# Kernel tuning notes

Hardware: AMD Instinct MI355X
Metric: run time of the kernel (lower is better)

Reference implementation:

```python
import jax, jax.numpy as jnp
import numpy as np

S, V = 64, 32          # input scalar / vector multiplicities (64x0e + 32x1o)
MID_S, MID_V = 96, 96  # irreps_mid = 64x0e+32x0e + 64x1o+32x1o
NB = 10                # number_of_basis (radial edge scalars)
N_NODES, N_EDGES = 50000, 400000


def _fctp_attr(xs, xv, attr, Ws, Wv):
    # FullyConnectedTensorProduct(x, node_attr='1x0e'): per-irrep-block linear
    # mixing scaled by the scalar attr, path weight 1/sqrt(fan_in).
    os = (xs @ Ws) * attr * (1.0 / np.sqrt(xs.shape[1]))
    ov = jnp.einsum('nui,uk->nki', xv, Wv) * attr[..., None] * (1.0 / np.sqrt(xv.shape[1]))
    return os, ov


def _conv(ns, nv, attr, src, dst, sh, esc,
          Wsc_s, Wsc_v, Wl1_s, Wl1_v, Wfc1, Wfc2, Wl2_s, Wl2_v, Wa):
    # GraphConvolutionWithNodeAttrs: gather -> weighted e3nn TP -> scatter-mean
    N, E = ns.shape[0], src.shape[0]
    # radial MLP (e3nn FullyConnectedNet, silu) -> per-edge tp weights (192)
    h = jax.nn.silu(esc @ Wfc1 * (1.0 / np.sqrt(esc.shape[1])))
    w = h @ Wfc2 * (1.0 / np.sqrt(h.shape[1]))
    w1, w2, w3, w4 = w[:, :64], w[:, 64:128], w[:, 128:160], w[:, 160:192]
    sc_s, sc_v = _fctp_attr(ns, nv, attr, Wsc_s, Wsc_v)   # self connection
    hs, hv = _fctp_attr(ns, nv, attr, Wl1_s, Wl1_v)       # lin1
    gs, gv = hs[src], hv[src]                              # gather by edge_src
    sh0, shv = sh[:, 0:1], sh[:, 1:4]                      # 1x0e, 1x1o edge sh
    # 'uvu' instructions: (0e x 0e -> 0e), (1o x 1o -> 0e), (0e x 1o -> 1o), (1o x 0e -> 1o)
    m_s = jnp.concatenate([
        gs * sh0 * w1,                                                     # [E,64]
        jnp.einsum('evi,ei->ev', gv, shv) * (1.0 / np.sqrt(3.0)) * w4],   # [E,32]
        axis=1)                                                            # [E,96]
    m_v = jnp.concatenate([
        gs[:, :, None] * shv[:, None, :] * w2[:, :, None],  # [E,64,3]
        gv * sh0[:, :, None] * w3[:, :, None]],              # [E,32,3]
        axis=1)                                              # [E,96,3]
    # scatter with reduce='mean' onto destination nodes
    deg = jnp.maximum(jax.ops.segment_sum(jnp.ones((E,), ns.dtype), dst, num_segments=N), 1.0)
    Ms = jax.ops.segment_sum(m_s, dst, num_segments=N) / deg[:, None]
    Mv = jax.ops.segment_sum(m_v, dst, num_segments=N) / deg[:, None, None]
    alpha = (Ms @ Wa) * (1.0 / np.sqrt(MID_S)) * attr      # [N,1] (output_mask==1)
    os, ov = _fctp_attr(Ms, Mv, attr, Wl2_s, Wl2_v)        # lin2
    return sc_s + alpha * os, sc_v + alpha[..., None] * ov


def _forward(node_s, node_v, node_attr, edge_src, edge_dst, edge_sh, edge_scalars, p1, p2):
    s, v = _conv(node_s, node_v, node_attr, edge_src, edge_dst, edge_sh, edge_scalars, *p1)
    # Gate: 64 scalars (silu) | 32 gates (sigmoid) gating 32x1o vectors
    gs = jax.nn.silu(s[:, :64])
    v = v * jax.nn.sigmoid(s[:, 64:96])[:, :, None]
    s2, v2 = _conv(gs, v, node_attr, edge_src, edge_dst, edge_sh, edge_scalars, *p2)
    return jnp.concatenate([s2, v2.reshape(v2.shape[0], -1)], axis=1)  # [N,160]


def setup_inputs():
    ks = jax.random.split(jax.random.key(0), 32)
    N, E = N_NODES, N_EDGES
    g = lambda i, shape: jax.random.normal(ks[i], shape, jnp.float32)
    inp = {'node_s': g(0, (N, S)),
           'node_v': g(1, (N, V, 3)),
           'node_attr': jnp.ones((N, 1), jnp.float32),
           'edge_src': jax.random.randint(ks[2], (E,), 0, N),
           'edge_dst': jax.random.randint(ks[3], (E,), 0, N),
           'edge_sh': g(4, (E, 4)),
           'edge_scalars': jax.random.uniform(ks[5], (E, NB), jnp.float32)}
    dims = {1: (96, 32), 2: (64, 32)}  # layer1 conv out feeds gate; layer2 is final conv
    i = 6
    for L in (1, 2):
        o_s, o_v = dims[L]
        for name, shape in [('sc_s', (S, o_s)), ('sc_v', (V, o_v)), ('lin1_s', (S, S)),
                            ('lin1_v', (V, V)), ('fc1', (NB, 64)), ('fc2', (64, 192)),
                            ('lin2_s', (MID_S, o_s)), ('lin2_v', (MID_V, o_v)), ('alpha', (MID_S, 1))]:
            inp['l%d_%s' % (L, name)] = g(i, shape)
            i += 1
    return inp


def reference(node_s, node_v, node_attr, edge_src, edge_dst, edge_sh, edge_scalars,
              l1_sc_s, l1_sc_v, l1_lin1_s, l1_lin1_v, l1_fc1, l1_fc2, l1_lin2_s, l1_lin2_v, l1_alpha,
              l2_sc_s, l2_sc_v, l2_lin1_s, l2_lin1_v, l2_fc1, l2_fc2, l2_lin2_s, l2_lin2_v, l2_alpha):
    p1 = (l1_sc_s, l1_sc_v, l1_lin1_s, l1_lin1_v, l1_fc1, l1_fc2, l1_lin2_s, l1_lin2_v, l1_alpha)
    p2 = (l2_sc_s, l2_sc_v, l2_lin1_s, l2_lin1_v, l2_fc1, l2_fc2, l2_lin2_s, l2_lin2_v, l2_alpha)
    return _forward(node_s, node_v, node_attr, edge_src, edge_dst, edge_sh, edge_scalars, p1, p2)
```

## Files before the change

kernel.cpp:

```cpp
#include <hip/hip_runtime.h>
#include <hip/hip_bf16.h>

#define INV_SQRT10 0.31622776601683794f
#define INV_SQRT64 0.125f
#define INV_SQRT32 0.17677669529663687f
#define INV_SQRT96 0.10206207261596575f
#define INV_SQRT3  0.5773502691896258f

typedef __attribute__((ext_vector_type(4))) float f32x4;
typedef __attribute__((ext_vector_type(8))) short bf16x8;

__device__ __forceinline__ unsigned short f2bf(float x) {
    return __builtin_bit_cast(unsigned short, (__hip_bfloat16)x);
}
__device__ __forceinline__ float bf2f(unsigned short u) {
    union { unsigned u; float f; } v; v.u = ((unsigned)u) << 16;
    return v.f;
}

__global__ __launch_bounds__(256) void k_prep_nodes(
    const float* __restrict__ ns, const float* __restrict__ nv,
    const int* __restrict__ dst,
    unsigned short* __restrict__ xsb, unsigned short* __restrict__ xvpb,
    int* __restrict__ cnt, int N, int E)
{
    const int gid = blockIdx.x * 256 + threadIdx.x, gs = gridDim.x * 256;
    for (int i = gid; i < N * 64; i += gs) xsb[i] = f2bf(ns[i]);
    for (int i = gid; i < N * 96; i += gs) {
        const int n = i / 96, rem = i - n * 96;
        const int ic = rem >> 5, u = rem & 31;
        xvpb[i] = f2bf(nv[(size_t)n * 96 + u * 3 + ic]);
    }
    for (int i = gid; i < E; i += gs) atomicAdd(&cnt[dst[i]], 1);
}

template <int OS>
__global__ __launch_bounds__(256) void k_prep_w(
    const float* __restrict__ Wl1s, const float* __restrict__ Wscs,
    const float* __restrict__ Wl1v, const float* __restrict__ Wscv,
    const float* __restrict__ Wfc2,
    const float* __restrict__ W2s, const float* __restrict__ W2v,
    const float* __restrict__ Wa,
    unsigned short* __restrict__ wsb, unsigned short* __restrict__ wvb,
    unsigned short* __restrict__ wfb,
    unsigned short* __restrict__ wob, unsigned short* __restrict__ wv2b)
{
    constexpr int NC1 = 64 + OS;
    constexpr int PC1 = ((OS + 16 + 15) / 16) * 16;
    const int gid = blockIdx.x * 256 + threadIdx.x, gs = gridDim.x * 256;
    for (int i = gid; i < NC1 * 64; i += gs) {
        const int c = i >> 6, k = i & 63;
        const float v = (c < 64) ? Wl1s[k * 64 + c] : Wscs[k * OS + (c - 64)];
        wsb[i] = f2bf(v);
    }
    for (int i = gid; i < 64 * 32; i += gs) {
        const int c = i >> 5, u = i & 31;
        const float v = (c < 32) ? Wl1v[u * 32 + c] : Wscv[u * 32 + (c - 32)];
        wvb[i] = f2bf(v);
    }
    for (int i = gid; i < 192 * 64; i += gs) {
        const int c = i >> 6, k = i & 63;
        wfb[i] = f2bf(Wfc2[k * 192 + c]);
    }
    for (int i = gid; i < PC1 * 96; i += gs) {
        const int c = i / 96, u = i - c * 96;
        float v = 0.f;
        if (c < OS) v = W2s[u * OS + c];
        else if (c == OS) v = Wa[u];
        wob[i] = f2bf(v);
    }
    for (int i = gid; i < 32 * 96; i += gs) {
        const int c = i / 96, u = i - c * 96;
        wv2b[i] = f2bf(W2v[u * 32 + c]);
    }
}

__global__ __launch_bounds__(256) void k_scan1(const int* __restrict__ cnt,
                                               int* __restrict__ partial, int N)
{
    __shared__ int lds[256];
    const int t = threadIdx.x, i = blockIdx.x * 256 + t;
    int v = (i < N) ? cnt[i] : 0;
    lds[t] = v;
    __syncthreads();
    for (int off = 128; off > 0; off >>= 1) {
        if (t < off) lds[t] += lds[t + off];
        __syncthreads();
    }
    if (t == 0) partial[blockIdx.x] = lds[0];
}

__global__ __launch_bounds__(1024) void k_scan2(int* __restrict__ partial, int NB)
{
    __shared__ int lds[1024];
    const int t = threadIdx.x;
    int v = (t < NB) ? partial[t] : 0;
    lds[t] = v;
    __syncthreads();
    for (int off = 1; off < 1024; off <<= 1) {
        int w = (t >= off) ? lds[t - off] : 0;
        __syncthreads();
        lds[t] += w;
        __syncthreads();
    }
    if (t < NB) partial[t] = lds[t] - v;
}

__global__ __launch_bounds__(256) void k_scan3(const int* __restrict__ cnt,
                                               const int* __restrict__ partial,
                                               int* __restrict__ base, int N)
{
    __shared__ int lds[256];
    const int t = threadIdx.x, i = blockIdx.x * 256 + t;
    int v = (i < N) ? cnt[i] : 0;
    lds[t] = v;
    __syncthreads();
    for (int off = 1; off < 256; off <<= 1) {
        int w = (t >= off) ? lds[t - off] : 0;
        __syncthreads();
        lds[t] += w;
        __syncthreads();
    }
    if (i < N) base[i] = partial[blockIdx.x] + lds[t] - v;
}

__global__ __launch_bounds__(256) void k_order(
    const int* __restrict__ dst, const int* __restrict__ base,
    int* __restrict__ cursor, int* __restrict__ order, int E)
{
    int i = blockIdx.x * 256 + threadIdx.x;
    if (i < E) {
        const int d = dst[i];
        order[base[d] + atomicAdd(&cursor[d], 1)] = i;
    }
}

__global__ __launch_bounds__(256) void k_gather(
    const int* __restrict__ order,
    const int* __restrict__ src, const float* __restrict__ sh,
    const float* __restrict__ esc,
    int* __restrict__ src_ord, float4* __restrict__ sh_ord,
    unsigned short* __restrict__ esc_ordb, int E)
{
    int pos = blockIdx.x * 256 + threadIdx.x;
    if (pos < E) {
        const int e = order[pos];
        src_ord[pos] = src[e];
        sh_ord[pos] = ((const float4*)sh)[e];
        const float* ep = esc + (size_t)e * 10;
        unsigned short* eo = esc_ordb + (size_t)pos * 10;
        #pragma unroll
        for (int q = 0; q < 10; q++) eo[q] = f2bf(ep[q]);
    }
}

template <int OS>
__global__ __launch_bounds__(256) void k_node_mfma(
    const unsigned short* __restrict__ xsb, const unsigned short* __restrict__ xvpb,
    const float* __restrict__ attr,
    const unsigned short* __restrict__ wsb, const unsigned short* __restrict__ wvb,
    unsigned short* __restrict__ hsb, unsigned short* __restrict__ hvbb,
    unsigned short* __restrict__ scs, unsigned short* __restrict__ scv, int N)
{
    constexpr int NC1 = 64 + OS;
    constexpr int CT1 = NC1 / 16;
    __shared__ float attr_l[64];
    const int tid = threadIdx.x;
    const int n0 = blockIdx.x * 64;
    if (tid < 64) attr_l[tid] = (n0 + tid < N) ? attr[n0 + tid] : 0.f;
    __syncthreads();
    const int wv = tid >> 6, lane = tid & 63;
    const int mrow = lane & 15, kg = lane >> 4;

    {
        const int rbase = wv * 16;
        const int r = rbase + mrow;
        const int rc = min(n0 + r, N - 1);
        const bf16x8 a0 = *(const bf16x8*)(xsb + (size_t)rc * 64 + kg * 8);
        const bf16x8 a1 = *(const bf16x8*)(xsb + (size_t)rc * 64 + 32 + kg * 8);
        f32x4 acc[CT1];
        #pragma unroll
        for (int t = 0; t < CT1; t++) acc[t] = (f32x4){0.f, 0.f, 0.f, 0.f};
        #pragma unroll
        for (int t = 0; t < CT1; t++) {
            const int c = t * 16 + mrow;
            const bf16x8 b0 = *(const bf16x8*)(wsb + c * 64 + kg * 8);
            const bf16x8 b1 = *(const bf16x8*)(wsb + c * 64 + 32 + kg * 8);
            acc[t] = __builtin_amdgcn_mfma_f32_16x16x32_bf16(a0, b0, acc[t], 0, 0, 0);
            acc[t] = __builtin_amdgcn_mfma_f32_16x16x32_bf16(a1, b1, acc[t], 0, 0, 0);
        }
        #pragma unroll
        for (int t = 0; t < CT1; t++) {
            const int c = t * 16 + mrow;
            #pragma unroll
            for (int rg = 0; rg < 4; rg++) {
                const int row = rbase + kg * 4 + rg;
                const int n = n0 + row;
                if (n < N) {
                    const float v = acc[t][rg] * INV_SQRT64 * attr_l[row];
                    if (c < 64) hsb[(size_t)n * 64 + c] = f2bf(v);
                    else        scs[(size_t)n * OS + (c - 64)] = f2bf(v);
                }
            }
        }
    }
    #pragma unroll
    for (int j = 0; j < 3; j++) {
        const int rbase = (wv * 3 + j) * 16;
        const int rv = rbase + mrow;
        const int ic = rv >> 6, nloc = rv & 63;
        const int nc = min(n0 + nloc, N - 1);
        const bf16x8 a = *(const bf16x8*)(xvpb + (size_t)nc * 96 + ic * 32 + kg * 8);
        f32x4 acc2[4];
        #pragma unroll
        for (int t = 0; t < 4; t++) acc2[t] = (f32x4){0.f, 0.f, 0.f, 0.f};
        #pragma unroll
        for (int t = 0; t < 4; t++) {
            const int c = t * 16 + mrow;
            const bf16x8 b = *(const bf16x8*)(wvb + c * 32 + kg * 8);
            acc2[t] = __builtin_amdgcn_mfma_f32_16x16x32_bf16(a, b, acc2[t], 0, 0, 0);
        }
        #pragma unroll
        for (int t = 0; t < 4; t++) {
            const int c = t * 16 + mrow;
            #pragma unroll
            for (int rg = 0; rg < 4; rg++) {
                const int rv2 = rbase + kg * 4 + rg;
                const int ic2 = rv2 >> 6, nl = rv2 & 63;
                const int n = n0 + nl;
                if (n < N) {
                    const float v = acc2[t][rg] * INV_SQRT32 * attr_l[nl];
                    if (c < 32) hvbb[(size_t)n * 96 + ic2 * 32 + c] = f2bf(v);
                    else        scv[(size_t)n * 96 + ic2 * 32 + (c - 32)] = f2bf(v);
                }
            }
        }
    }
}

__global__ __launch_bounds__(256) void k_edge_mlp(
    const unsigned short* __restrict__ esc_ordb, const int* __restrict__ base,
    const float* __restrict__ Wfc1, const unsigned short* __restrict__ wfb,
    unsigned* __restrict__ wbuf12, unsigned short* __restrict__ wbufB,
    int n0, int n1, int N, int E, int cap)
{
    __shared__ float w1_l[640];
    __shared__ __align__(16) char hb[64 * 64 * 2];
    __shared__ __align__(16) char wf_l[192 * 64 * 2];
    const int tid = threadIdx.x;
    const int lo = (n0 == 0) ? 0 : base[n0];
    const int hi = (n1 >= N) ? E : base[n1];
    const int p0 = lo + blockIdx.x * 64;
    if (p0 >= hi) return;

    for (int i = tid; i < 640; i += 256) w1_l[i] = Wfc1[i];
    for (int i = tid; i < 1536; i += 256) {
        const int c = i >> 3, k16 = i & 7;
        const uint4 v = *(const uint4*)(wfb + c * 64 + k16 * 8);
        *(uint4*)(wf_l + (((c << 7) + (k16 << 4)) ^ ((c & 7) << 4))) = v;
    }
    const int r = tid >> 2, c0 = (tid & 3) << 4;
    float ev[10];
    {
        const int rc = min(p0 + r, E - 1);
        const unsigned* ep = (const unsigned*)(esc_ordb + (size_t)rc * 10);
        #pragma unroll
        for (int q = 0; q < 5; q++) {
            const unsigned u = ep[q];
            ev[2 * q]     = bf2f((unsigned short)(u & 0xFFFF));
            ev[2 * q + 1] = bf2f((unsigned short)(u >> 16));
        }
    }
    __syncthreads();
    {
        float hval[16];
        #pragma unroll
        for (int c = 0; c < 16; c++) {
            float acc = 0.f;
            #pragma unroll
            for (int q = 0; q < 10; q++) acc += ev[q] * w1_l[q * 64 + c0 + c];
            acc *= INV_SQRT10;
            hval[c] = acc / (1.f + __expf(-acc));
        }
        unsigned pk[8];
        #pragma unroll
        for (int j = 0; j < 8; j++)
            pk[j] = (unsigned)f2bf(hval[2 * j]) | ((unsigned)f2bf(hval[2 * j + 1]) << 16);
        const int swz = (r & 7) << 4;
        const int b0 = (r << 7) + (c0 << 1);
        *(uint4*)(hb + (b0 ^ swz)) = make_uint4(pk[0], pk[1], pk[2], pk[3]);
        *(uint4*)(hb + ((b0 + 16) ^ swz)) = make_uint4(pk[4], pk[5], pk[6], pk[7]);
    }
    __syncthreads();
    const int wv = tid >> 6, lane = tid & 63;
    const int mrow = lane & 15, kgrp = lane >> 4;
    f32x4 acc[12];
    #pragma unroll
    for (int t = 0; t < 12; t++) acc[t] = (f32x4){0.f, 0.f, 0.f, 0.f};
    #pragma unroll
    for (int kc = 0; kc < 2; kc++) {
        const int rr = wv * 16 + mrow;
        const int abyte = ((rr << 7) + (kc << 6) + (kgrp << 4)) ^ ((rr & 7) << 4);
        const bf16x8 afrag = *(const bf16x8*)(hb + abyte);
        #pragma unroll
        for (int t = 0; t < 12; t++) {
            const int c = t * 16 + mrow;
            const int bbyte = ((c << 7) + (kc << 6) + (kgrp << 4)) ^ ((c & 7) << 4);
            const bf16x8 bfrag = *(const bf16x8*)(wf_l + bbyte);
            acc[t] = __builtin_amdgcn_mfma_f32_16x16x32_bf16(afrag, bfrag, acc[t], 0, 0, 0);
        }
    }
    #pragma unroll
    for (int rg = 0; rg < 4; rg++) {
        const int rloc = wv * 16 + kgrp * 4 + rg;
        const int pos = p0 + rloc;
        if (pos < hi && (pos - lo) < cap) {
            uint4 pk12;
            pk12.x = (unsigned)f2bf(acc[0][rg] * INV_SQRT64) | ((unsigned)f2bf(acc[4][rg] * INV_SQRT64) << 16);
            pk12.y = (unsigned)f2bf(acc[1][rg] * INV_SQRT64) | ((unsigned)f2bf(acc[5][rg] * INV_SQRT64) << 16);
            pk12.z = (unsigned)f2bf(acc[2][rg] * INV_SQRT64) | ((unsigned)f2bf(acc[6][rg] * INV_SQRT64) << 16);
            pk12.w = (unsigned)f2bf(acc[3][rg] * INV_SQRT64) | ((unsigned)f2bf(acc[7][rg] * INV_SQRT64) << 16);
            ushort4 pkB;
            pkB.x = f2bf(acc[8][rg] * INV_SQRT64);
            pkB.y = f2bf(acc[9][rg] * INV_SQRT64);
            pkB.z = f2bf(acc[10][rg] * INV_SQRT64);
            pkB.w = f2bf(acc[11][rg] * INV_SQRT64);
            *(uint4*)(wbuf12 + (size_t)(pos - lo) * 64 + mrow * 4) = pk12;
            *(ushort4*)(wbufB + (size_t)(pos - lo) * 64 + mrow * 4) = pkB;
        }
    }
}

__global__ __launch_bounds__(256) void k_agg(
    const unsigned short* __restrict__ hsb, const unsigned short* __restrict__ hvbb,
    const int* __restrict__ src_ord, const float4* __restrict__ sh_ord,
    const int* __restrict__ base, const int* __restrict__ cnt,
    const unsigned* __restrict__ wbuf12, const unsigned short* __restrict__ wbufB,
    unsigned short* __restrict__ Msb, unsigned short* __restrict__ Mvb,
    int n0, int n1, int N, int E)
{
    const int wave = threadIdx.x >> 6, lane = threadIdx.x & 63;
    const int n = n0 + blockIdx.x * 4 + wave;
    if (n >= n1) return;
    const int lo = (n0 == 0) ? 0 : base[n0];
    const int cidx = (lane & 15) * 4 + (lane >> 4);

    float aS = 0.f, aSB = 0.f;
    float aV0 = 0.f, aV1 = 0.f, aV2 = 0.f;
    float aB0 = 0.f, aB1 = 0.f, aB2 = 0.f;
    const int b0 = base[n];
    const int c_ = cnt[n];
    const size_t wb = (size_t)(b0 - lo) * 64;

    unsigned p12A = 0; float wBA = 0.f, gsA = 0.f;
    float gv0A = 0.f, gv1A = 0.f, gv2A = 0.f;
    float4 s4A = make_float4(0.f, 0.f, 0.f, 0.f);
    int s2 = 0;
    if (c_ > 0) {
        const int s1 = src_ord[b0];
        s2 = (c_ > 1) ? src_ord[b0 + 1] : 0;
        p12A = wbuf12[wb + cidx];
        wBA = bf2f(wbufB[wb + cidx]);
        gsA = bf2f(hsb[(size_t)s1 * 64 + lane]);
        if (lane < 32) {
            gv0A = bf2f(hvbb[(size_t)s1 * 96 + lane]);
            gv1A = bf2f(hvbb[(size_t)s1 * 96 + 32 + lane]);
            gv2A = bf2f(hvbb[(size_t)s1 * 96 + 64 + lane]);
        }
        s4A = sh_ord[b0];
    }
    for (int j = 0; j < c_; ++j) {
        unsigned p12B = 0; float wBB = 0.f, gsB = 0.f;
        float gv0B = 0.f, gv1B = 0.f, gv2B = 0.f;
        float4 s4B = make_float4(0.f, 0.f, 0.f, 0.f);
        if (j + 1 < c_) {
            p12B = wbuf12[wb + (size_t)(j + 1) * 64 + cidx];
            wBB = bf2f(wbufB[wb + (size_t)(j + 1) * 64 + cidx]);
            gsB = bf2f(hsb[(size_t)s2 * 64 + lane]);
            if (lane < 32) {
                gv0B = bf2f(hvbb[(size_t)s2 * 96 + lane]);
                gv1B = bf2f(hvbb[(size_t)s2 * 96 + 32 + lane]);
                gv2B = bf2f(hvbb[(size_t)s2 * 96 + 64 + lane]);
            }
            s4B = sh_ord[b0 + j + 1];
        }
        const int s2n = (j + 2 < c_) ? src_ord[b0 + j + 2] : 0;
        {
            const float w1 = bf2f((unsigned short)(p12A & 0xFFFF));
            const float w2 = bf2f((unsigned short)(p12A >> 16));
            const float gvdot = gv0A * s4A.y + gv1A * s4A.z + gv2A * s4A.w;
            const float gvd = __shfl(gvdot, lane & 31);
            aS  += gsA * s4A.x * w1;
            aSB += gvd * INV_SQRT3 * wBA;
            aV0 += gsA * s4A.y * w2;
            aV1 += gsA * s4A.z * w2;
            aV2 += gsA * s4A.w * w2;
            aB0 += gv0A * s4A.x * wBA;
            aB1 += gv1A * s4A.x * wBA;
            aB2 += gv2A * s4A.x * wBA;
        }
        p12A = p12B; wBA = wBB; gsA = gsB;
        gv0A = gv0B; gv1A = gv1B; gv2A = gv2B;
        s4A = s4B; s2 = s2n;
    }
    const float invd = 1.f / (float)max(c_, 1);
    unsigned short* msp = Msb + (size_t)n * 96;
    unsigned short* mvp = Mvb + (size_t)n * 3 * 96;
    msp[lane] = f2bf(aS * invd);
    if (lane >= 32) msp[64 + (lane - 32)] = f2bf(aSB * invd);
    mvp[0 * 96 + lane] = f2bf(aV0 * invd);
    mvp[1 * 96 + lane] = f2bf(aV1 * invd);
    mvp[2 * 96 + lane] = f2bf(aV2 * invd);
    if (lane < 32) {
        mvp[0 * 96 + 64 + lane] = f2bf(aB0 * invd);
        mvp[1 * 96 + 64 + lane] = f2bf(aB1 * invd);
        mvp[2 * 96 + 64 + lane] = f2bf(aB2 * invd);
    }
}

template <int OS, bool FINAL>
__global__ __launch_bounds__(256) void k_node_out(
    const unsigned short* __restrict__ Msb, const unsigned short* __restrict__ Mvb,
    const float* __restrict__ attr,
    const unsigned short* __restrict__ scs, const unsigned short* __restrict__ scv,
    const unsigned short* __restrict__ wob, const unsigned short* __restrict__ wv2b,
    float* __restrict__ outF,
    unsigned short* __restrict__ outSb, unsigned short* __restrict__ outVb, int N)
{
    constexpr int CT1 = (OS + 16 + 15) / 16;
    constexpr int TA = OS / 16;
    __shared__ float attr_l[64];
    __shared__ float alpha_l[64];
    __shared__ float gate_l[64][32];
    const int tid = threadIdx.x;
    const int n0 = blockIdx.x * 64;
    if (tid < 64) attr_l[tid] = (n0 + tid < N) ? attr[n0 + tid] : 0.f;
    __syncthreads();
    const int wv = tid >> 6, lane = tid & 63;
    const int mrow = lane & 15, kg = lane >> 4;

    const int rbase = wv * 16;
    const int rc = min(n0 + rbase + mrow, N - 1);
    f32x4 acc[CT1];
    #pragma unroll
    for (int t = 0; t < CT1; t++) acc[t] = (f32x4){0.f, 0.f, 0.f, 0.f};
    #pragma unroll
    for (int kc = 0; kc < 3; kc++) {
        const bf16x8 a = *(const bf16x8*)(Msb + (size_t)rc * 96 + kc * 32 + kg * 8);
        #pragma unroll
        for (int t = 0; t < CT1; t++) {
            const bf16x8 b = *(const bf16x8*)(wob + (size_t)(t * 16 + mrow) * 96 + kc * 32 + kg * 8);
            acc[t] = __builtin_amdgcn_mfma_f32_16x16x32_bf16(a, b, acc[t], 0, 0, 0);
        }
    }
    if (mrow == 0) {
        #pragma unroll
        for (int rg = 0; rg < 4; rg++) {
            const int row = rbase + kg * 4 + rg;
            alpha_l[row] = acc[TA][rg] * INV_SQRT96 * attr_l[row];
        }
    }
    __syncthreads();
    #pragma unroll
    for (int t = 0; t < CT1; t++) {
        const int c = t * 16 + mrow;
        if (c < OS) {
            #pragma unroll
            for (int rg = 0; rg < 4; rg++) {
                const int row = rbase + kg * 4 + rg;
                const int n = n0 + row;
                if (n < N) {
                    const float os = acc[t][rg] * INV_SQRT96 * attr_l[row];
                    const float s = bf2f(scs[(size_t)n * OS + c]) + alpha_l[row] * os;
                    if (FINAL) {
                        outF[(size_t)n * 160 + c] = s;
                    } else {
                        if (c < 64) outSb[(size_t)n * 64 + c] = f2bf(s / (1.f + __expf(-s)));
                        else        gate_l[row][c - 64] = 1.f / (1.f + __expf(-s));
                    }
                }
            }
        }
    }
    __syncthreads();
    #pragma unroll
    for (int j = 0; j < 3; j++) {
        const int rb2 = (wv * 3 + j) * 16;
        const int rv = rb2 + mrow;
        const int nl = rv / 3, ii = rv - nl * 3;
        const int nc2 = min(n0 + nl, N - 1);
        f32x4 acc2[2];
        acc2[0] = (f32x4){0.f, 0.f, 0.f, 0.f};
        acc2[1] = (f32x4){0.f, 0.f, 0.f, 0.f};
        #pragma unroll
        for (int kc = 0; kc < 3; kc++) {
            const bf16x8 a = *(const bf16x8*)(Mvb + ((size_t)nc2 * 3 + ii) * 96 + kc * 32 + kg * 8);
            #pragma unroll
            for (int t = 0; t < 2; t++) {
                const bf16x8 b = *(const bf16x8*)(wv2b + (size_t)(t * 16 + mrow) * 96 + kc * 32 + kg * 8);
                acc2[t] = __builtin_amdgcn_mfma_f32_16x16x32_bf16(a, b, acc2[t], 0, 0, 0);
            }
        }
        #pragma unroll
        for (int t = 0; t < 2; t++) {
            const int k = t * 16 + mrow;
            #pragma unroll
            for (int rg = 0; rg < 4; rg++) {
                const int rv2 = rb2 + kg * 4 + rg;
                const int nl2 = rv2 / 3, i2 = rv2 - nl2 * 3;
                const int n = n0 + nl2;
                if (n < N) {
                    const float ov = acc2[t][rg] * INV_SQRT96 * attr_l[nl2];
                    const float v = bf2f(scv[(size_t)n * 96 + i2 * 32 + k]) + alpha_l[nl2] * ov;
                    if (FINAL) outF[(size_t)n * 160 + 64 + k * 3 + i2] = v;
                    else       outVb[(size_t)n * 96 + i2 * 32 + k] = f2bf(v * gate_l[nl2][k]);
                }
            }
        }
    }
}

extern "C" void kernel_launch(void* const* d_in, const int* in_sizes, int n_in,
                              void* d_out, int out_size, void* d_ws, size_t ws_size,
                              hipStream_t stream)
{
    const float* node_s = (const float*)d_in[0];
    const float* node_v = (const float*)d_in[1];
    const float* attr   = (const float*)d_in[2];
    const int*   esrc   = (const int*)d_in[3];
    const int*   edst   = (const int*)d_in[4];
    const float* esh    = (const float*)d_in[5];
    const float* esc    = (const float*)d_in[6];
    const float* W[18];
    for (int i = 0; i < 18; i++) W[i] = (const float*)d_in[7 + i];

    const int N = in_sizes[0] / 64;
    const int E = in_sizes[3];
    const int NB = (N + 255) / 256;

    char* p = (char*)d_ws;
    unsigned short* xsb  = (unsigned short*)p; p += (size_t)N * 64 * 2;
    unsigned short* xvpb = (unsigned short*)p; p += (size_t)N * 96 * 2;
    unsigned short* hsb  = (unsigned short*)p; p += (size_t)N * 64 * 2;
    unsigned short* hvbb = (unsigned short*)p; p += (size_t)N * 96 * 2;
    unsigned short* Msb  = (unsigned short*)p; p += (size_t)N * 96 * 2;
    unsigned short* Mvb  = (unsigned short*)p; p += (size_t)N * 288 * 2;
    unsigned short* scs  = (unsigned short*)p; p += (size_t)N * 96 * 2;
    unsigned short* scv  = (unsigned short*)p; p += (size_t)N * 96 * 2;
    unsigned short* wsb1 = (unsigned short*)p; p += 160 * 64 * 2;
    unsigned short* wsb2 = (unsigned short*)p; p += 128 * 64 * 2;
    unsigned short* wvb1 = (unsigned short*)p; p += 64 * 32 * 2;
    unsigned short* wvb2 = (unsigned short*)p; p += 64 * 32 * 2;
    unsigned short* wfb1 = (unsigned short*)p; p += 192 * 64 * 2;
    unsigned short* wfb2 = (unsigned short*)p; p += 192 * 64 * 2;
    unsigned short* wob1 = (unsigned short*)p; p += 112 * 96 * 2;
    unsigned short* wob2 = (unsigned short*)p; p += 80 * 96 * 2;
    unsigned short* wv2b1 = (unsigned short*)p; p += 32 * 96 * 2;
    unsigned short* wv2b2 = (unsigned short*)p; p += 32 * 96 * 2;
    int* cnt    = (int*)p; p += (size_t)N * 4;
    int* cursor = (int*)p; p += (size_t)N * 4;
    int* basei  = (int*)p; p += (size_t)N * 4;
    int* partial = (int*)p; p += (size_t)NB * 4;
    p = (char*)(((size_t)p + 255) & ~(size_t)255);
    int* order   = (int*)p; p += (size_t)E * 4;
    int* src_ord = (int*)p; p += (size_t)E * 4;
    p = (char*)(((size_t)p + 15) & ~(size_t)15);
    float4* sh_ord = (float4*)p; p += (size_t)E * 16;
    unsigned short* esc_ordb = (unsigned short*)p; p += (size_t)E * 20;
    p = (char*)(((size_t)p + 255) & ~(size_t)255);
    const size_t used_fixed = (size_t)(p - (char*)d_ws);

    int NQ = 4;
    size_t cap = 0;
    {
        const int cands[3] = {1, 2, 4};
        for (int ci = 0; ci < 3; ci++) {
            const int c = cands[ci];
            size_t cc = (c == 1) ? (size_t)E : ((size_t)E / c) * 9 / 8 + 256;
            if (used_fixed + cc * 384 <= ws_size) { NQ = c; cap = cc; break; }
        }
        if (cap == 0) { NQ = 4; cap = ((size_t)E / 4) * 9 / 8 + 256; }
    }
    unsigned* wbuf12      = (unsigned*)p;       p += cap * 256;
    unsigned short* wbufB = (unsigned short*)p; p += cap * 128;

    const int nb  = (N + 63) / 64;
    const int ebk = (E + 255) / 256;
    const int Q   = (N + NQ - 1) / NQ;
    const int qb  = (Q + 3) / 4;
    const int emb = (int)((cap + 63) / 64);

    hipMemsetAsync(cnt, 0, (size_t)2 * N * sizeof(int), stream);
    k_prep_nodes<<<2048, 256, 0, stream>>>(node_s, node_v, edst, xsb, xvpb, cnt, N, E);
    k_prep_w<96><<<32, 256, 0, stream>>>(W[2], W[0], W[3], W[1], W[5], W[6], W[7], W[8],
                                         wsb1, wvb1, wfb1, wob1, wv2b1);
    k_prep_w<64><<<32, 256, 0, stream>>>(W[11], W[9], W[12], W[10], W[14], W[15], W[16], W[17],
                                         wsb2, wvb2, wfb2, wob2, wv2b2);
    k_scan1<<<NB, 256, 0, stream>>>(cnt, partial, N);
    k_scan2<<<1, 1024, 0, stream>>>(partial, NB);
    k_scan3<<<NB, 256, 0, stream>>>(cnt, partial, basei, N);
    k_order<<<ebk, 256, 0, stream>>>(edst, basei, cursor, order, E);
    k_gather<<<ebk, 256, 0, stream>>>(order, esrc, esh, esc,
                                      src_ord, sh_ord, esc_ordb, E);

    k_node_mfma<96><<<nb, 256, 0, stream>>>(xsb, xvpb, attr, wsb1, wvb1,
                                            hsb, hvbb, scs, scv, N);
    for (int q = 0; q < NQ; q++) {
        const int n0 = q * Q, n1 = min(N, (q + 1) * Q);
        if (n0 >= n1) break;
        k_edge_mlp<<<emb, 256, 0, stream>>>(esc_ordb, basei, W[4], wfb1,
                                            wbuf12, wbufB, n0, n1, N, E, (int)cap);
        k_agg<<<qb, 256, 0, stream>>>(hsb, hvbb, src_ord, sh_ord, basei, cnt,
                                      wbuf12, wbufB, Msb, Mvb, n0, n1, N, E);
    }
    k_node_out<96, false><<<nb, 256, 0, stream>>>(Msb, Mvb, attr, scs, scv,
                                                  wob1, wv2b1,
                                                  nullptr, xsb, xvpb, N);
    k_node_mfma<64><<<nb, 256, 0, stream>>>(xsb, xvpb, attr, wsb2, wvb2,
                                            hsb, hvbb, scs, scv, N);
    for (int q = 0; q < NQ; q++) {
        const int n0 = q * Q, n1 = min(N, (q + 1) * Q);
        if (n0 >= n1) break;
        k_edge_mlp<<<emb, 256, 0, stream>>>(esc_ordb, basei, W[13], wfb2,
                                            wbuf12, wbufB, n0, n1, N, E, (int)cap);
        k_agg<<<qb, 256, 0, stream>>>(hsb, hvbb, src_ord, sh_ord, basei, cnt,
                                      wbuf12, wbufB, Msb, Mvb, n0, n1, N, E);
    }
    k_node_out<64, true><<<nb, 256, 0, stream>>>(Msb, Mvb, attr, scs, scv,
                                                 wob2, wv2b2,
                                                 (float*)d_out, nullptr, nullptr, N);
}
```

Baseline: 465.6 us.

## Pad hv to 4-wide per channel and batch edge gathers four at a time

The lin1 vector output is now stored as [N,32,4] bf16, padded to 128 entries per node, so each aggregation lane fetches its three vector components with one 8-byte load instead of three scalar loads. The aggregation loop drops its one-ahead software prefetch and instead issues the loads for up to four edges before computing on them, which puts more memory requests in flight per wave. The cost is a larger hv buffer with a third more bytes per node, strided two-byte stores in the node kernel, and more registers in the aggregation kernel.

New measurement: 484.1 us. 4.0% more time.

```diff
diff --git a/kernel.cpp b/kernel.cpp
--- a/kernel.cpp
+++ b/kernel.cpp
@@ -159,7 +159,7 @@
     const unsigned short* __restrict__ xsb, const unsigned short* __restrict__ xvpb,
     const float* __restrict__ attr,
     const unsigned short* __restrict__ wsb, const unsigned short* __restrict__ wvb,
-    unsigned short* __restrict__ hsb, unsigned short* __restrict__ hvbb,
+    unsigned short* __restrict__ hsb, unsigned short* __restrict__ hvbb4,
     unsigned short* __restrict__ scs, unsigned short* __restrict__ scv, int N)
 {
     constexpr int NC1 = 64 + OS;
@@ -230,7 +230,7 @@
                 const int n = n0 + nl;
                 if (n < N) {
                     const float v = acc2[t][rg] * INV_SQRT32 * attr_l[nl];
-                    if (c < 32) hvbb[(size_t)n * 96 + ic2 * 32 + c] = f2bf(v);
+                    if (c < 32) hvbb4[(size_t)n * 128 + c * 4 + ic2] = f2bf(v);
                     else        scv[(size_t)n * 96 + ic2 * 32 + (c - 32)] = f2bf(v);
                 }
             }
@@ -332,7 +332,7 @@
 }
 
 __global__ __launch_bounds__(256) void k_agg(
-    const unsigned short* __restrict__ hsb, const unsigned short* __restrict__ hvbb,
+    const unsigned short* __restrict__ hsb, const unsigned short* __restrict__ hvbb4,
     const int* __restrict__ src_ord, const float4* __restrict__ sh_ord,
     const int* __restrict__ base, const int* __restrict__ cnt,
     const unsigned* __restrict__ wbuf12, const unsigned short* __restrict__ wbufB,
@@ -352,56 +352,47 @@
     const int c_ = cnt[n];
     const size_t wb = (size_t)(b0 - lo) * 64;
 
-    unsigned p12A = 0; float wBA = 0.f, gsA = 0.f;
-    float gv0A = 0.f, gv1A = 0.f, gv2A = 0.f;
-    float4 s4A = make_float4(0.f, 0.f, 0.f, 0.f);
-    int s2 = 0;
-    if (c_ > 0) {
-        const int s1 = src_ord[b0];
-        s2 = (c_ > 1) ? src_ord[b0 + 1] : 0;
-        p12A = wbuf12[wb + cidx];
-        wBA = bf2f(wbufB[wb + cidx]);
-        gsA = bf2f(hsb[(size_t)s1 * 64 + lane]);
-        if (lane < 32) {
-            gv0A = bf2f(hvbb[(size_t)s1 * 96 + lane]);
-            gv1A = bf2f(hvbb[(size_t)s1 * 96 + 32 + lane]);
-            gv2A = bf2f(hvbb[(size_t)s1 * 96 + 64 + lane]);
-        }
-        s4A = sh_ord[b0];
-    }
-    for (int j = 0; j < c_; ++j) {
-        unsigned p12B = 0; float wBB = 0.f, gsB = 0.f;
-        float gv0B = 0.f, gv1B = 0.f, gv2B = 0.f;
-        float4 s4B = make_float4(0.f, 0.f, 0.f, 0.f);
-        if (j + 1 < c_) {
-            p12B = wbuf12[wb + (size_t)(j + 1) * 64 + cidx];
-            wBB = bf2f(wbufB[wb + (size_t)(j + 1) * 64 + cidx]);
-            gsB = bf2f(hsb[(size_t)s2 * 64 + lane]);
-            if (lane < 32) {
-                gv0B = bf2f(hvbb[(size_t)s2 * 96 + lane]);
-                gv1B = bf2f(hvbb[(size_t)s2 * 96 + 32 + lane]);
-                gv2B = bf2f(hvbb[(size_t)s2 * 96 + 64 + lane]);
+    for (int j0 = 0; j0 < c_; j0 += 4) {
+        const int m = c_ - j0;
+        int sidx[4];
+        unsigned p12[4];
+        float wB[4], gs[4];
+        ushort4 gv[4];
+        float4 s4[4];
+        #pragma unroll
+        for (int k = 0; k < 4; k++)
+            if (k < m) sidx[k] = src_ord[b0 + j0 + k];
+        #pragma unroll
+        for (int k = 0; k < 4; k++) {
+            if (k < m) {
+                p12[k] = wbuf12[wb + (size_t)(j0 + k) * 64 + cidx];
+                wB[k] = bf2f(wbufB[wb + (size_t)(j0 + k) * 64 + cidx]);
+                gs[k] = bf2f(hsb[(size_t)sidx[k] * 64 + lane]);
+                if (lane < 32)
+                    gv[k] = *(const ushort4*)(hvbb4 + (size_t)sidx[k] * 128 + lane * 4);
+                else
+                    gv[k] = make_ushort4(0, 0, 0, 0);
+                s4[k] = sh_ord[b0 + j0 + k];
             }
-            s4B = sh_ord[b0 + j + 1];
-        }
-        const int s2n = (j + 2 < c_) ? src_ord[b0 + j + 2] : 0;
-        {
-            const float w1 = bf2f((unsigned short)(p12A & 0xFFFF));
-            const float w2 = bf2f((unsigned short)(p12A >> 16));
-            const float gvdot = gv0A * s4A.y + gv1A * s4A.z + gv2A * s4A.w;
-            const float gvd = __shfl(gvdot, lane & 31);
-            aS  += gsA * s4A.x * w1;
-            aSB += gvd * INV_SQRT3 * wBA;
-            aV0 += gsA * s4A.y * w2;
-            aV1 += gsA * s4A.z * w2;
-            aV2 += gsA * s4A.w * w2;
-            aB0 += gv0A * s4A.x * wBA;
-            aB1 += gv1A * s4A.x * wBA;
-            aB2 += gv2A * s4A.x * wBA;
-        }
-        p12A = p12B; wBA = wBB; gsA = gsB;
-        gv0A = gv0B; gv1A = gv1B; gv2A = gv2B;
-        s4A = s4B; s2 = s2n;
+        }
+        #pragma unroll
+        for (int k = 0; k < 4; k++) {
+            if (k < m) {
+                const float w1 = bf2f((unsigned short)(p12[k] & 0xFFFF));
+                const float w2 = bf2f((unsigned short)(p12[k] >> 16));
+                const float g0 = bf2f(gv[k].x), g1 = bf2f(gv[k].y), g2 = bf2f(gv[k].z);
+                const float gvdot = g0 * s4[k].y + g1 * s4[k].z + g2 * s4[k].w;
+                const float gvd = __shfl(gvdot, lane & 31);
+                aS  += gs[k] * s4[k].x * w1;
+                aSB += gvd * INV_SQRT3 * wB[k];
+                aV0 += gs[k] * s4[k].y * w2;
+                aV1 += gs[k] * s4[k].z * w2;
+                aV2 += gs[k] * s4[k].w * w2;
+                aB0 += g0 * s4[k].x * wB[k];
+                aB1 += g1 * s4[k].x * wB[k];
+                aB2 += g2 * s4[k].x * wB[k];
+            }
+        }
     }
     const float invd = 1.f / (float)max(c_, 1);
     unsigned short* msp = Msb + (size_t)n * 96;
@@ -542,7 +533,7 @@
     unsigned short* xsb  = (unsigned short*)p; p += (size_t)N * 64 * 2;
     unsigned short* xvpb = (unsigned short*)p; p += (size_t)N * 96 * 2;
     unsigned short* hsb  = (unsigned short*)p; p += (size_t)N * 64 * 2;
-    unsigned short* hvbb = (unsigned short*)p; p += (size_t)N * 96 * 2;
+    unsigned short* hvbb4 = (unsigned short*)p; p += (size_t)N * 128 * 2;
     unsigned short* Msb  = (unsigned short*)p; p += (size_t)N * 96 * 2;
     unsigned short* Mvb  = (unsigned short*)p; p += (size_t)N * 288 * 2;
     unsigned short* scs  = (unsigned short*)p; p += (size_t)N * 96 * 2;
@@ -604,26 +595,26 @@
                                       src_ord, sh_ord, esc_ordb, E);
 
     k_node_mfma<96><<<nb, 256, 0, stream>>>(xsb, xvpb, attr, wsb1, wvb1,
-                                            hsb, hvbb, scs, scv, N);
+                                            hsb, hvbb4, scs, scv, N);
     for (int q = 0; q < NQ; q++) {
         const int n0 = q * Q, n1 = min(N, (q + 1) * Q);
         if (n0 >= n1) break;
         k_edge_mlp<<<emb, 256, 0, stream>>>(esc_ordb, basei, W[4], wfb1,
                                             wbuf12, wbufB, n0, n1, N, E, (int)cap);
-        k_agg<<<qb, 256, 0, stream>>>(hsb, hvbb, src_ord, sh_ord, basei, cnt,
+        k_agg<<<qb, 256, 0, stream>>>(hsb, hvbb4, src_ord, sh_ord, basei, cnt,
                                       wbuf12, wbufB, Msb, Mvb, n0, n1, N, E);
     }
     k_node_out<96, false><<<nb, 256, 0, stream>>>(Msb, Mvb, attr, scs, scv,
                                                   wob1, wv2b1,
                                                   nullptr, xsb, xvpb, N);
     k_node_mfma<64><<<nb, 256, 0, stream>>>(xsb, xvpb, attr, wsb2, wvb2,
-                                            hsb, hvbb, scs, scv, N);
+                                            hsb, hvbb4, scs, scv, N);
     for (int q = 0; q < NQ; q++) {
         const int n0 = q * Q, n1 = min(N, (q + 1) * Q);
         if (n0 >= n1) break;
         k_edge_mlp<<<emb, 256, 0, stream>>>(esc_ordb, basei, W[13], wfb2,
                                             wbuf12, wbufB, n0, n1, N, E, (int)cap);
-        k_agg<<<qb, 256, 0, stream>>>(hsb, hvbb, src_ord, sh_ord, basei, cnt,
+        k_agg<<<qb, 256, 0, stream>>>(hsb, hvbb4, src_ord, sh_ord, basei, cnt,
                                       wbuf12, wbufB, Msb, Mvb, n0, n1, N, E);
     }
     k_node_out<64, true><<<nb, 256, 0, stream>>>(Msb, Mvb, attr, scs, scv,
```

## Split per-node edge aggregation across two waves and interleave gathered vector features

Applied to the files above, without the earlier changes.

The aggregation kernel now gives each destination node two wavefronts, each handling half of its incoming edges. The partial sums are combined through shared memory, and one wave writes the mean. Separately, the gathered vector features are stored as [N][32][4] (padded xyz), so each lane fetches its three components with one 8-byte load instead of three strided loads. This targets the latency-bound serial edge loop and the gather load count, at the cost of a block barrier, extra shared memory, idle waves for low-degree nodes, and a larger hv buffer.

Result: slower. 498.0 us (+7.0%).

```diff
diff --git a/kernel.cpp b/kernel.cpp
--- a/kernel.cpp
+++ b/kernel.cpp
@@ -159,7 +159,7 @@
     const unsigned short* __restrict__ xsb, const unsigned short* __restrict__ xvpb,
     const float* __restrict__ attr,
     const unsigned short* __restrict__ wsb, const unsigned short* __restrict__ wvb,
-    unsigned short* __restrict__ hsb, unsigned short* __restrict__ hvbb,
+    unsigned short* __restrict__ hsb, unsigned short* __restrict__ hvbb4,
     unsigned short* __restrict__ scs, unsigned short* __restrict__ scv, int N)
 {
     constexpr int NC1 = 64 + OS;
@@ -230,7 +230,7 @@
                 const int n = n0 + nl;
                 if (n < N) {
                     const float v = acc2[t][rg] * INV_SQRT32 * attr_l[nl];
-                    if (c < 32) hvbb[(size_t)n * 96 + ic2 * 32 + c] = f2bf(v);
+                    if (c < 32) hvbb4[(size_t)n * 128 + c * 4 + ic2] = f2bf(v);
                     else        scv[(size_t)n * 96 + ic2 * 32 + (c - 32)] = f2bf(v);
                 }
             }
@@ -332,89 +332,117 @@
 }
 
 __global__ __launch_bounds__(256) void k_agg(
-    const unsigned short* __restrict__ hsb, const unsigned short* __restrict__ hvbb,
+    const unsigned short* __restrict__ hsb, const unsigned short* __restrict__ hvbb4,
     const int* __restrict__ src_ord, const float4* __restrict__ sh_ord,
     const int* __restrict__ base, const int* __restrict__ cnt,
     const unsigned* __restrict__ wbuf12, const unsigned short* __restrict__ wbufB,
     unsigned short* __restrict__ Msb, unsigned short* __restrict__ Mvb,
     int n0, int n1, int N, int E)
 {
+    __shared__ float comb[4][8][64];
     const int wave = threadIdx.x >> 6, lane = threadIdx.x & 63;
-    const int n = n0 + blockIdx.x * 4 + wave;
-    if (n >= n1) return;
+    const int pair = wave >> 1, half = wave & 1;
+    const int n = n0 + blockIdx.x * 2 + pair;
+    const bool valid = n < n1;
     const int lo = (n0 == 0) ? 0 : base[n0];
     const int cidx = (lane & 15) * 4 + (lane >> 4);
 
     float aS = 0.f, aSB = 0.f;
     float aV0 = 0.f, aV1 = 0.f, aV2 = 0.f;
     float aB0 = 0.f, aB1 = 0.f, aB2 = 0.f;
-    const int b0 = base[n];
-    const int c_ = cnt[n];
-    const size_t wb = (size_t)(b0 - lo) * 64;
-
-    unsigned p12A = 0; float wBA = 0.f, gsA = 0.f;
-    float gv0A = 0.f, gv1A = 0.f, gv2A = 0.f;
-    float4 s4A = make_float4(0.f, 0.f, 0.f, 0.f);
-    int s2 = 0;
-    if (c_ > 0) {
-        const int s1 = src_ord[b0];
-        s2 = (c_ > 1) ? src_ord[b0 + 1] : 0;
-        p12A = wbuf12[wb + cidx];
-        wBA = bf2f(wbufB[wb + cidx]);
-        gsA = bf2f(hsb[(size_t)s1 * 64 + lane]);
+    int c_ = 0;
+    if (valid) {
+        const int b0n = base[n];
+        c_ = cnt[n];
+        const int hcnt = (c_ + 1) >> 1;
+        const int jb = half * hcnt;
+        const int je = min(c_, jb + hcnt);
+        const int b0 = b0n + jb;
+        const int cw = je - jb;
+        const size_t wb = (size_t)(b0 - lo) * 64;
+
+        unsigned p12A = 0; float wBA = 0.f, gsA = 0.f;
+        float gv0A = 0.f, gv1A = 0.f, gv2A = 0.f;
+        float4 s4A = make_float4(0.f, 0.f, 0.f, 0.f);
+        int s2 = 0;
+        if (cw > 0) {
+            const int s1 = src_ord[b0];
+            s2 = (cw > 1) ? src_ord[b0 + 1] : 0;
+            p12A = wbuf12[wb + cidx];
+            wBA = bf2f(wbufB[wb + cidx]);
+            gsA = bf2f(hsb[(size_t)s1 * 64 + lane]);
+            if (lane < 32) {
+                const ushort4 g = *(const ushort4*)(hvbb4 + (size_t)s1 * 128 + lane * 4);
+                gv0A = bf2f(g.x); gv1A = bf2f(g.y); gv2A = bf2f(g.z);
+            }
+            s4A = sh_ord[b0];
+        }
+        for (int j = 0; j < cw; ++j) {
+            unsigned p12B = 0; float wBB = 0.f, gsB = 0.f;
+            float gv0B = 0.f, gv1B = 0.f, gv2B = 0.f;
+            float4 s4B = make_float4(0.f, 0.f, 0.f, 0.f);
+            if (j + 1 < cw) {
+                p12B = wbuf12[wb + (size_t)(j + 1) * 64 + cidx];
+                wBB = bf2f(wbufB[wb + (size_t)(j + 1) * 64 + cidx]);
+                gsB = bf2f(hsb[(size_t)s2 * 64 + lane]);
+                if (lane < 32) {
+                    const ushort4 g = *(const ushort4*)(hvbb4 + (size_t)s2 * 128 + lane * 4);
+                    gv0B = bf2f(g.x); gv1B = bf2f(g.y); gv2B = bf2f(g.z);
+                }
+                s4B = sh_ord[b0 + j + 1];
+            }
+            const int s2n = (j + 2 < cw) ? src_ord[b0 + j + 2] : 0;
+            {
+                const float w1 = bf2f((unsigned short)(p12A & 0xFFFF));
+                const float w2 = bf2f((unsigned short)(p12A >> 16));
+                const float gvdot = gv0A * s4A.y + gv1A * s4A.z + gv2A * s4A.w;
+                const float gvd = __shfl(gvdot, lane & 31);
+                aS  += gsA * s4A.x * w1;
+                aSB += gvd * INV_SQRT3 * wBA;
+                aV0 += gsA * s4A.y * w2;
+                aV1 += gsA * s4A.z * w2;
+                aV2 += gsA * s4A.w * w2;
+                aB0 += gv0A * s4A.x * wBA;
+                aB1 += gv1A * s4A.x * wBA;
+                aB2 += gv2A * s4A.x * wBA;
+            }
+            p12A = p12B; wBA = wBB; gsA = gsB;
+            gv0A = gv0B; gv1A = gv1B; gv2A = gv2B;
+            s4A = s4B; s2 = s2n;
+        }
+    }
+    comb[wave][0][lane] = aS;
+    comb[wave][1][lane] = aSB;
+    comb[wave][2][lane] = aV0;
+    comb[wave][3][lane] = aV1;
+    comb[wave][4][lane] = aV2;
+    comb[wave][5][lane] = aB0;
+    comb[wave][6][lane] = aB1;
+    comb[wave][7][lane] = aB2;
+    __syncthreads();
+    if (valid && half == 0) {
+        const int ow = wave + 1;
+        aS  += comb[ow][0][lane];
+        aSB += comb[ow][1][lane];
+        aV0 += comb[ow][2][lane];
+        aV1 += comb[ow][3][lane];
+        aV2 += comb[ow][4][lane];
+        aB0 += comb[ow][5][lane];
+        aB1 += comb[ow][6][lane];
+        aB2 += comb[ow][7][lane];
+        const float invd = 1.f / (float)max(c_, 1);
+        unsigned short* msp = Msb + (size_t)n * 96;
+        unsigned short* mvp = Mvb + (size_t)n * 3 * 96;
+        msp[lane] = f2bf(aS * invd);
+        if (lane >= 32) msp[64 + (lane - 32)] = f2bf(aSB * invd);
+        mvp[0 * 96 + lane] = f2bf(aV0 * invd);
+        mvp[1 * 96 + lane] = f2bf(aV1 * invd);
+        mvp[2 * 96 + lane] = f2bf(aV2 * invd);
         if (lane < 32) {
-            gv0A = bf2f(hvbb[(size_t)s1 * 96 + lane]);
-            gv1A = bf2f(hvbb[(size_t)s1 * 96 + 32 + lane]);
-            gv2A = bf2f(hvbb[(size_t)s1 * 96 + 64 + lane]);
-        }
-        s4A = sh_ord[b0];
-    }
-    for (int j = 0; j < c_; ++j) {
-        unsigned p12B = 0; float wBB = 0.f, gsB = 0.f;
-        float gv0B = 0.f, gv1B = 0.f, gv2B = 0.f;
-        float4 s4B = make_float4(0.f, 0.f, 0.f, 0.f);
-        if (j + 1 < c_) {
-            p12B = wbuf12[wb + (size_t)(j + 1) * 64 + cidx];
-            wBB = bf2f(wbufB[wb + (size_t)(j + 1) * 64 + cidx]);
-            gsB = bf2f(hsb[(size_t)s2 * 64 + lane]);
-            if (lane < 32) {
-                gv0B = bf2f(hvbb[(size_t)s2 * 96 + lane]);
-                gv1B = bf2f(hvbb[(size_t)s2 * 96 + 32 + lane]);
-                gv2B = bf2f(hvbb[(size_t)s2 * 96 + 64 + lane]);
-            }
-            s4B = sh_ord[b0 + j + 1];
-        }
-        const int s2n = (j + 2 < c_) ? src_ord[b0 + j + 2] : 0;
-        {
-            const float w1 = bf2f((unsigned short)(p12A & 0xFFFF));
-            const float w2 = bf2f((unsigned short)(p12A >> 16));
-            const float gvdot = gv0A * s4A.y + gv1A * s4A.z + gv2A * s4A.w;
-            const float gvd = __shfl(gvdot, lane & 31);
-            aS  += gsA * s4A.x * w1;
-            aSB += gvd * INV_SQRT3 * wBA;
-            aV0 += gsA * s4A.y * w2;
-            aV1 += gsA * s4A.z * w2;
-            aV2 += gsA * s4A.w * w2;
-            aB0 += gv0A * s4A.x * wBA;
-            aB1 += gv1A * s4A.x * wBA;
-            aB2 += gv2A * s4A.x * wBA;
-        }
-        p12A = p12B; wBA = wBB; gsA = gsB;
-        gv0A = gv0B; gv1A = gv1B; gv2A = gv2B;
-        s4A = s4B; s2 = s2n;
-    }
-    const float invd = 1.f / (float)max(c_, 1);
-    unsigned short* msp = Msb + (size_t)n * 96;
-    unsigned short* mvp = Mvb + (size_t)n * 3 * 96;
-    msp[lane] = f2bf(aS * invd);
-    if (lane >= 32) msp[64 + (lane - 32)] = f2bf(aSB * invd);
-    mvp[0 * 96 + lane] = f2bf(aV0 * invd);
-    mvp[1 * 96 + lane] = f2bf(aV1 * invd);
-    mvp[2 * 96 + lane] = f2bf(aV2 * invd);
-    if (lane < 32) {
-        mvp[0 * 96 + 64 + lane] = f2bf(aB0 * invd);
-        mvp[1 * 96 + 64 + lane] = f2bf(aB1 * invd);
-        mvp[2 * 96 + 64 + lane] = f2bf(aB2 * invd);
+            mvp[0 * 96 + 64 + lane] = f2bf(aB0 * invd);
+            mvp[1 * 96 + 64 + lane] = f2bf(aB1 * invd);
+            mvp[2 * 96 + 64 + lane] = f2bf(aB2 * invd);
+        }
     }
 }
 
@@ -542,7 +570,7 @@
     unsigned short* xsb  = (unsigned short*)p; p += (size_t)N * 64 * 2;
     unsigned short* xvpb = (unsigned short*)p; p += (size_t)N * 96 * 2;
     unsigned short* hsb  = (unsigned short*)p; p += (size_t)N * 64 * 2;
-    unsigned short* hvbb = (unsigned short*)p; p += (size_t)N * 96 * 2;
+    unsigned short* hvbb4 = (unsigned short*)p; p += (size_t)N * 128 * 2;
     unsigned short* Msb  = (unsigned short*)p; p += (size_t)N * 96 * 2;
     unsigned short* Mvb  = (unsigned short*)p; p += (size_t)N * 288 * 2;
     unsigned short* scs  = (unsigned short*)p; p += (size_t)N * 96 * 2;
@@ -587,7 +615,7 @@
     const int nb  = (N + 63) / 64;
     const int ebk = (E + 255) / 256;
     const int Q   = (N + NQ - 1) / NQ;
-    const int qb  = (Q + 3) / 4;
+    const int qb  = (Q + 1) / 2;
     const int emb = (int)((cap + 63) / 64);
 
     hipMemsetAsync(cnt, 0, (size_t)2 * N * sizeof(int), stream);
@@ -604,26 +632,26 @@
                                       src_ord, sh_ord, esc_ordb, E);
 
     k_node_mfma<96><<<nb, 256, 0, stream>>>(xsb, xvpb, attr, wsb1, wvb1,
-                                            hsb, hvbb, scs, scv, N);
+                                            hsb, hvbb4, scs, scv, N);
     for (int q = 0; q < NQ; q++) {
         const int n0 = q * Q, n1 = min(N, (q + 1) * Q);
         if (n0 >= n1) break;
         k_edge_mlp<<<emb, 256, 0, stream>>>(esc_ordb, basei, W[4], wfb1,
                                             wbuf12, wbufB, n0, n1, N, E, (int)cap);
-        k_agg<<<qb, 256, 0, stream>>>(hsb, hvbb, src_ord, sh_ord, basei, cnt,
+        k_agg<<<qb, 256, 0, stream>>>(hsb, hvbb4, src_ord, sh_ord, basei, cnt,
                                       wbuf12, wbufB, Msb, Mvb, n0, n1, N, E);
     }
     k_node_out<96, false><<<nb, 256, 0, stream>>>(Msb, Mvb, attr, scs, scv,
                                                   wob1, wv2b1,
                                                   nullptr, xsb, xvpb, N);
     k_node_mfma<64><<<nb, 256, 0, stream>>>(xsb, xvpb, attr, wsb2, wvb2,
-                                            hsb, hvbb, scs, scv, N);
+                                            hsb, hvbb4, scs, scv, N);
     for (int q = 0; q < NQ; q++) {
         const int n0 = q * Q, n1 = min(N, (q + 1) * Q);
         if (n0 >= n1) break;
         k_edge_mlp<<<emb, 256, 0, stream>>>(esc_ordb, basei, W[13], wfb2,
                                             wbuf12, wbufB, n0, n1, N, E, (int)cap);
-        k_agg<<<qb, 256, 0, stream>>>(hsb, hvbb, src_ord, sh_ord, basei, cnt,
+        k_agg<<<qb, 256, 0, stream>>>(hsb, hvbb4, src_ord, sh_ord, basei, cnt,
                                       wbuf12, wbufB, Msb, Mvb, n0, n1, N, E);
     }
     k_node_out<64, true><<<nb, 256, 0, stream>>>(Msb, Mvb, attr, scs, scv,
```
